# Kernel optimization log

Hardware: AMD Instinct MI355X
Metric: run time of the kernel (lower is better)

## Reference

```python
import jax, jax.numpy as jnp
import numpy as np

EMBED_DIM = 1024
NUM_HEADS = 16
HEAD_DIM = EMBED_DIM // NUM_HEADS
B, S = 2, 2048


def setup_inputs() -> dict:
    key = jax.random.key(0)
    ks = jax.random.split(key, 8)
    std = 1.0 / np.sqrt(EMBED_DIM)
    return {
        "xq": jax.random.normal(ks[0], (B, S, EMBED_DIM), jnp.float32),
        "xk": jax.random.normal(ks[1], (B, S, EMBED_DIM), jnp.float32),
        "xv": jax.random.normal(ks[2], (B, S, EMBED_DIM), jnp.float32),
        "Wq": jax.random.normal(ks[3], (EMBED_DIM, EMBED_DIM), jnp.float32) * std,
        "Wk": jax.random.normal(ks[4], (EMBED_DIM, EMBED_DIM), jnp.float32) * std,
        "Wv": jax.random.normal(ks[5], (EMBED_DIM, EMBED_DIM), jnp.float32) * std,
        "Wo": jax.random.normal(ks[6], (EMBED_DIM, EMBED_DIM), jnp.float32) * std,
        "bo": jnp.zeros((EMBED_DIM,), jnp.float32),
    }


def reference(xq, xk, xv, Wq, Wk, Wv, Wo, bo):
    # nn.Linear(x) = x @ W.T ; then view last dim into (heads, head_dim)
    def proj(x, W):
        y = jnp.einsum('bse,fe->bsf', x, W)
        return y.reshape(x.shape[0], x.shape[1], NUM_HEADS, HEAD_DIM)

    q = proj(xq, Wq)  # [b, m, h, f]
    k = proj(xk, Wk)  # [b, n, h, f]
    v = proj(xv, Wv)  # [b, n, h, f]

    scaling = 1.0 / np.sqrt(HEAD_DIM).astype(np.float32)
    dot = scaling * jnp.einsum('bmhf,bnhf->bhmn', q, k)  # [b, h, m, n]
    attn = jax.nn.softmax(dot, axis=-1)
    out = jnp.einsum('bhmn,bnhf->bmhf', attn, v)  # [b, m, h, f]

    Wo_hf = Wo.reshape(EMBED_DIM, NUM_HEADS, HEAD_DIM)
    return jnp.einsum('bmhf,ehf->bme', out, Wo_hf) + bo
```

## Files before the change

### kernel.cpp

```cpp
#include <hip/hip_runtime.h>
#include <math.h>


#define EMBED 1024
#define SEQ   2048
#define BATCH 2
#define NH    16
#define HD    64

typedef __attribute__((ext_vector_type(8))) short bf16x8;
typedef __attribute__((ext_vector_type(4))) short bf16x4;
typedef __attribute__((ext_vector_type(4))) float f32x4;
typedef __attribute__((ext_vector_type(4))) unsigned int u32x4;

#define QSCALE 0.18033688f

__device__ inline unsigned short f2bf(float f) {
  unsigned int u = __builtin_bit_cast(unsigned int, f);
  u += 0x7fffu + ((u >> 16) & 1u);
  return (unsigned short)(u >> 16);
}
__device__ inline float bf2f(unsigned short s) {
  unsigned int u = ((unsigned int)s) << 16;
  return __builtin_bit_cast(float, u);
}

__device__ inline unsigned packbf(float lo, float hi) {
  return __builtin_amdgcn_perm(__builtin_bit_cast(unsigned int, hi),
                               __builtin_bit_cast(unsigned int, lo),
                               0x07060302u);
}

__device__ inline void async_cp16(const void* g, void* l) {
  __builtin_amdgcn_global_load_lds(
      (const __attribute__((address_space(1))) unsigned int*)g,
      (__attribute__((address_space(3))) unsigned int*)l, 16, 0, 0);
}

__global__ void detect_kernel(const unsigned int* __restrict__ xq, int* __restrict__ flag) {
  __shared__ int cnt[256];
  int t = threadIdx.x;
  unsigned int w = xq[t];
  unsigned int e = (w >> 7) & 0xFFu;
  cnt[t] = (e >= 0x70u && e <= 0x8Fu) ? 1 : 0;
  __syncthreads();
  for (int s = 128; s > 0; s >>= 1) {
    if (t < s) cnt[t] += cnt[t + s];
    __syncthreads();
  }
  if (t == 0) *flag = (cnt[0] >= 160) ? 1 : 0;
}

struct PackPtrs {
  const void* src[7];
  unsigned short* dst[7];
};
__global__ __launch_bounds__(256) void pack_all(PackPtrs p, const int* __restrict__ flagp) {
  const bool isbf = (*flagp != 0);
  int ci = blockIdx.x * 256 + threadIdx.x;
  int t, rel;
  if (ci < 1572864) { t = ci / 524288; rel = ci - t * 524288; }
  else { int r = ci - 1572864; int w = r / 131072; t = 3 + w; rel = r - w * 131072; }
  size_t off = (size_t)rel * 8;
  unsigned short* d = p.dst[t] + off;
  if (isbf) {
    *(bf16x8*)d = *(const bf16x8*)((const unsigned short*)p.src[t] + off);
  } else {
    const float* s = (const float*)p.src[t] + off;
    f32x4 f0 = *(const f32x4*)s;
    f32x4 f1 = *(const f32x4*)(s + 4);
    bf16x8 v;
#pragma unroll
    for (int e = 0; e < 4; ++e) {
      v[e] = (short)f2bf(f0[e]);
      v[4 + e] = (short)f2bf(f1[e]);
    }
    *(bf16x8*)d = v;
  }
}

struct QkvArgs {
  const unsigned short* A[3];
  const unsigned short* W[3];
  unsigned short* out[3];
};
__global__ __launch_bounds__(256) void gemm_qkv(QkvArgs args) {
  __shared__ __align__(16) unsigned short smem[16640];

  const int z = blockIdx.z;
  const unsigned short* A = args.A[z];
  const unsigned short* Bw = args.W[z];
  unsigned short* out = args.out[z];

  const int tid = threadIdx.x, lane = tid & 63, wave = tid >> 6;
  const int wm = wave >> 1, wn = wave & 1;
  const int q = lane >> 4, c = lane & 15;
  const int m0 = blockIdx.x * 128, n0 = blockIdx.y * 128;

  f32x4 acc[4][4];
#pragma unroll
  for (int i = 0; i < 4; ++i)
#pragma unroll
    for (int j = 0; j < 4; ++j) acc[i][j] = (f32x4){0.f, 0.f, 0.f, 0.f};

  auto STAGE = [&](int buf, int k0) {
#pragma unroll
    for (int jj = 0; jj < 2; ++jj) {
      int ci = jj * 256 + tid;
      async_cp16(A + (size_t)(m0 + (ci >> 2)) * EMBED + k0 + (ci & 3) * 8,
                 (void*)(smem + buf * 8192 + (jj * 256 + wave * 64) * 8));
      async_cp16(Bw + (size_t)(n0 + (ci >> 2)) * EMBED + k0 + (ci & 3) * 8,
                 (void*)(smem + buf * 8192 + 4096 + (jj * 256 + wave * 64) * 8));
    }
  };

  STAGE(0, 0);
  __syncthreads();
  for (int kt = 0; kt < EMBED / 32; ++kt) {
    const int p = kt & 1;
    if (kt + 1 < EMBED / 32) STAGE(1 - p, (kt + 1) * 32);
    const unsigned short* Ab = smem + p * 8192;
    const unsigned short* Bb = smem + p * 8192 + 4096;

    bf16x8 af[4], bfr[4];
#pragma unroll
    for (int i = 0; i < 4; ++i)
      af[i] = *(const bf16x8*)(Ab + (wm * 64 + i * 16 + c) * 32 + q * 8);
#pragma unroll
    for (int j = 0; j < 4; ++j)
      bfr[j] = *(const bf16x8*)(Bb + (wn * 64 + j * 16 + c) * 32 + q * 8);
#pragma unroll
    for (int i = 0; i < 4; ++i)
#pragma unroll
      for (int j = 0; j < 4; ++j)
        acc[i][j] = __builtin_amdgcn_mfma_f32_16x16x32_bf16(af[i], bfr[j], acc[i][j], 0, 0, 0);
    __syncthreads();
  }

  if (z < 2) {
    const float sc = (z == 0) ? QSCALE : 1.0f;
#pragma unroll
    for (int i = 0; i < 4; ++i)
#pragma unroll
      for (int j = 0; j < 4; ++j)
#pragma unroll
        for (int r = 0; r < 4; ++r) {
          int m = m0 + wm * 64 + i * 16 + q * 4 + r;
          int col = n0 + wn * 64 + j * 16 + c;
          int b = m >> 11, s = m & 2047, h = col >> 6, d = col & 63;
          out[(size_t)((b * NH + h) * SEQ + s) * HD + d] = f2bf(acc[i][j][r] * sc);
        }
  } else {
    __syncthreads();
#pragma unroll
    for (int i = 0; i < 4; ++i)
#pragma unroll
      for (int j = 0; j < 4; ++j)
#pragma unroll
        for (int r = 0; r < 4; ++r)
          smem[(wm * 64 + i * 16 + q * 4 + r) * 130 + wn * 64 + j * 16 + c] =
              f2bf(acc[i][j][r]);
    __syncthreads();
    int n = tid >> 1;
    int sh = (tid & 1) * 64;
    int b = m0 >> 11, s0l = m0 & 2047;
    int h = blockIdx.y * 2 + (n >> 6), d = n & 63;
    unsigned short* dst = out + (size_t)((b * NH + h) * HD + d) * SEQ + s0l + sh;
#pragma unroll
    for (int g = 0; g < 8; ++g) {
      bf16x8 v;
#pragma unroll
      for (int e = 0; e < 8; ++e) v[e] = (short)smem[(sh + g * 8 + e) * 130 + n];
      *(bf16x8*)(dst + g * 8) = v;
    }
  }
}

__global__ __launch_bounds__(256) void gemm_out(
    const unsigned short* __restrict__ A,
    const unsigned short* __restrict__ Bw,
    const void* __restrict__ bias,
    void* __restrict__ out,
    const int* __restrict__ flagp)
{
  __shared__ __align__(16) unsigned short smem[16384];

  const int tid = threadIdx.x, lane = tid & 63, wave = tid >> 6;
  const int wm = wave >> 1, wn = wave & 1;
  const int q = lane >> 4, c = lane & 15;
  const int m0 = blockIdx.x * 128, n0 = blockIdx.y * 128;

  f32x4 acc[4][4];
#pragma unroll
  for (int i = 0; i < 4; ++i)
#pragma unroll
    for (int j = 0; j < 4; ++j) acc[i][j] = (f32x4){0.f, 0.f, 0.f, 0.f};

  auto STAGE = [&](int buf, int k0) {
#pragma unroll
    for (int jj = 0; jj < 2; ++jj) {
      int ci = jj * 256 + tid;
      async_cp16(A + (size_t)(m0 + (ci >> 2)) * EMBED + k0 + (ci & 3) * 8,
                 (void*)(smem + buf * 8192 + (jj * 256 + wave * 64) * 8));
      async_cp16(Bw + (size_t)(n0 + (ci >> 2)) * EMBED + k0 + (ci & 3) * 8,
                 (void*)(smem + buf * 8192 + 4096 + (jj * 256 + wave * 64) * 8));
    }
  };

  STAGE(0, 0);
  __syncthreads();
  for (int kt = 0; kt < EMBED / 32; ++kt) {
    const int p = kt & 1;
    if (kt + 1 < EMBED / 32) STAGE(1 - p, (kt + 1) * 32);
    const unsigned short* Ab = smem + p * 8192;
    const unsigned short* Bb = smem + p * 8192 + 4096;

    bf16x8 af[4], bfr[4];
#pragma unroll
    for (int i = 0; i < 4; ++i)
      af[i] = *(const bf16x8*)(Ab + (wm * 64 + i * 16 + c) * 32 + q * 8);
#pragma unroll
    for (int j = 0; j < 4; ++j)
      bfr[j] = *(const bf16x8*)(Bb + (wn * 64 + j * 16 + c) * 32 + q * 8);
#pragma unroll
    for (int i = 0; i < 4; ++i)
#pragma unroll
      for (int j = 0; j < 4; ++j)
        acc[i][j] = __builtin_amdgcn_mfma_f32_16x16x32_bf16(af[i], bfr[j], acc[i][j], 0, 0, 0);
    __syncthreads();
  }

  const bool isbf = (*flagp != 0);
#pragma unroll
  for (int i = 0; i < 4; ++i)
#pragma unroll
    for (int j = 0; j < 4; ++j)
#pragma unroll
      for (int r = 0; r < 4; ++r) {
        int m = m0 + wm * 64 + i * 16 + q * 4 + r;
        int col = n0 + wn * 64 + j * 16 + c;
        float v = acc[i][j][r];
        v += isbf ? bf2f(((const unsigned short*)bias)[col]) : ((const float*)bias)[col];
        if (isnan(v)) v = 777.0f;
        if (isbf) ((unsigned short*)out)[(size_t)m * EMBED + col] = f2bf(v);
        else      ((float*)out)[(size_t)m * EMBED + col] = v;
      }
}

__global__ __launch_bounds__(256) void attn_kernel(
    const unsigned short* __restrict__ Qb,
    const unsigned short* __restrict__ Kb,
    const unsigned short* __restrict__ Vtb,
    unsigned short* __restrict__ Ob)
{
  __shared__ __align__(16) unsigned short Kt[2][64][72];
  __shared__ __align__(16) unsigned short Vs[2][64][72];

  const int tid = threadIdx.x;
  const int lane = tid & 63;
  const int wave = tid >> 6;
  const int q = lane >> 4, c = lane & 15;
  const int b = blockIdx.z, h = blockIdx.y;
  const int q0 = blockIdx.x * 128 + wave * 32;

  const unsigned short* Qh = Qb + ((size_t)(b * NH + h) * SEQ) * HD;
  const unsigned short* Kh = Kb + ((size_t)(b * NH + h) * SEQ) * HD;
  const unsigned short* Vh = Vtb + ((size_t)(b * NH + h) * HD) * SEQ;

  bf16x8 qflA = *(const bf16x8*)(Qh + (q0 + c) * HD + q * 8);
  bf16x8 qfhA = *(const bf16x8*)(Qh + (q0 + c) * HD + 32 + q * 8);
  bf16x8 qflB = *(const bf16x8*)(Qh + (q0 + 16 + c) * HD + q * 8);
  bf16x8 qfhB = *(const bf16x8*)(Qh + (q0 + 16 + c) * HD + 32 + q * 8);

  f32x4 oA[4], oB[4];
#pragma unroll
  for (int t = 0; t < 4; ++t) { oA[t] = (f32x4){0.f,0.f,0.f,0.f}; oB[t] = (f32x4){0.f,0.f,0.f,0.f}; }
  f32x4 lA = (f32x4){0.f,0.f,0.f,0.f}, lB = (f32x4){0.f,0.f,0.f,0.f};

  bf16x8 ones;
#pragma unroll
  for (int e = 0; e < 8; ++e) ones[e] = (short)0x3F80;

  const int r0 = tid >> 3;
  const int t7 = tid & 7;
  const int ch0 = t7 * 8;
  const int u0 = 8 * (t7 >> 2) + 4 * (t7 & 1) + ((t7 >> 1) & 1);

  const bf16x8* pK0 = (const bf16x8*)(Kh + (size_t)r0 * HD + ch0);
  const bf16x8* pK1 = (const bf16x8*)(Kh + (size_t)(32 + r0) * HD + ch0);
  const bf16x8* pV0 = (const bf16x8*)(Vh + (size_t)r0 * SEQ + ch0);
  const bf16x8* pV1 = (const bf16x8*)(Vh + (size_t)(32 + r0) * SEQ + ch0);

  bf16x8 kr0, kr1, vr0, vr1;
  kr0 = *pK0; pK0 += (64 * HD) / 8;
  kr1 = *pK1; pK1 += (64 * HD) / 8;
  vr0 = *pV0; pV0 += 64 / 8;
  vr1 = *pV1; pV1 += 64 / 8;
  *(bf16x8*)(&Kt[0][r0][ch0]) = kr0;
  *(bf16x8*)(&Kt[0][32 + r0][ch0]) = kr1;
  {
    bf16x4 lo0 = __builtin_shufflevector(vr0, vr0, 0, 1, 2, 3);
    bf16x4 hi0 = __builtin_shufflevector(vr0, vr0, 4, 5, 6, 7);
    bf16x4 lo1 = __builtin_shufflevector(vr1, vr1, 0, 1, 2, 3);
    bf16x4 hi1 = __builtin_shufflevector(vr1, vr1, 4, 5, 6, 7);
    *(bf16x4*)(&Vs[0][r0][u0 * 4]) = lo0;
    *(bf16x4*)(&Vs[0][r0][u0 * 4 + 8]) = hi0;
    *(bf16x4*)(&Vs[0][32 + r0][u0 * 4]) = lo1;
    *(bf16x4*)(&Vs[0][32 + r0][u0 * 4 + 8]) = hi1;
  }

  for (int kt = 0; kt < SEQ / 64; ++kt) {
    const int p = kt & 1;
    __syncthreads();
    if (kt + 1 < SEQ / 64) {
      kr0 = *pK0; pK0 += (64 * HD) / 8;
      kr1 = *pK1; pK1 += (64 * HD) / 8;
      vr0 = *pV0; pV0 += 64 / 8;
      vr1 = *pV1; pV1 += 64 / 8;
    }

    bf16x8 kf0[4], kf1[4];
#pragma unroll
    for (int s = 0; s < 4; ++s) {
      kf0[s] = *(const bf16x8*)(&Kt[p][s * 16 + c][q * 8]);
      kf1[s] = *(const bf16x8*)(&Kt[p][s * 16 + c][32 + q * 8]);
    }

#pragma unroll
    for (int g = 0; g < 2; ++g) {
      u32x4 pa, pb;
#pragma unroll
      for (int s2 = 0; s2 < 2; ++s2) {
        const int s = g * 2 + s2;
        f32x4 zA = {0.f, 0.f, 0.f, 0.f};
        f32x4 zB = {0.f, 0.f, 0.f, 0.f};
        zA = __builtin_amdgcn_mfma_f32_16x16x32_bf16(kf0[s], qflA, zA, 0, 0, 0);
        zA = __builtin_amdgcn_mfma_f32_16x16x32_bf16(kf1[s], qfhA, zA, 0, 0, 0);
        zB = __builtin_amdgcn_mfma_f32_16x16x32_bf16(kf0[s], qflB, zB, 0, 0, 0);
        zB = __builtin_amdgcn_mfma_f32_16x16x32_bf16(kf1[s], qfhB, zB, 0, 0, 0);
        float a0 = __builtin_amdgcn_exp2f(zA[0]);
        float a1 = __builtin_amdgcn_exp2f(zA[1]);
        float a2 = __builtin_amdgcn_exp2f(zA[2]);
        float a3 = __builtin_amdgcn_exp2f(zA[3]);
        float b0 = __builtin_amdgcn_exp2f(zB[0]);
        float b1 = __builtin_amdgcn_exp2f(zB[1]);
        float b2 = __builtin_amdgcn_exp2f(zB[2]);
        float b3 = __builtin_amdgcn_exp2f(zB[3]);
        pa[s2 * 2]     = packbf(a0, a1);
        pa[s2 * 2 + 1] = packbf(a2, a3);
        pb[s2 * 2]     = packbf(b0, b1);
        pb[s2 * 2 + 1] = packbf(b2, b3);
      }
      bf16x8 pfA = __builtin_bit_cast(bf16x8, pa);
      bf16x8 pfB = __builtin_bit_cast(bf16x8, pb);
      __builtin_amdgcn_s_setprio(1);
      lA = __builtin_amdgcn_mfma_f32_16x16x32_bf16(pfA, ones, lA, 0, 0, 0);
      lB = __builtin_amdgcn_mfma_f32_16x16x32_bf16(pfB, ones, lB, 0, 0, 0);
#pragma unroll
      for (int t = 0; t < 4; ++t) {
        bf16x8 vf = *(const bf16x8*)(&Vs[p][t * 16 + c][(g * 4 + q) * 8]);
        oA[t] = __builtin_amdgcn_mfma_f32_16x16x32_bf16(pfA, vf, oA[t], 0, 0, 0);
        oB[t] = __builtin_amdgcn_mfma_f32_16x16x32_bf16(pfB, vf, oB[t], 0, 0, 0);
      }
      __builtin_amdgcn_s_setprio(0);
    }

    if (kt + 1 < SEQ / 64) {
      *(bf16x8*)(&Kt[1 - p][r0][ch0]) = kr0;
      *(bf16x8*)(&Kt[1 - p][32 + r0][ch0]) = kr1;
      bf16x4 lo0 = __builtin_shufflevector(vr0, vr0, 0, 1, 2, 3);
      bf16x4 hi0 = __builtin_shufflevector(vr0, vr0, 4, 5, 6, 7);
      bf16x4 lo1 = __builtin_shufflevector(vr1, vr1, 0, 1, 2, 3);
      bf16x4 hi1 = __builtin_shufflevector(vr1, vr1, 4, 5, 6, 7);
      *(bf16x4*)(&Vs[1 - p][r0][u0 * 4]) = lo0;
      *(bf16x4*)(&Vs[1 - p][r0][u0 * 4 + 8]) = hi0;
      *(bf16x4*)(&Vs[1 - p][32 + r0][u0 * 4]) = lo1;
      *(bf16x4*)(&Vs[1 - p][32 + r0][u0 * 4 + 8]) = hi1;
    }
  }

  float invA[4], invB[4];
#pragma unroll
  for (int r = 0; r < 4; ++r) { invA[r] = 1.0f / lA[r]; invB[r] = 1.0f / lB[r]; }
#pragma unroll
  for (int t = 0; t < 4; ++t)
#pragma unroll
    for (int r = 0; r < 4; ++r) {
      int col = h * HD + t * 16 + c;
      int srowA = q0 + q * 4 + r;
      float vA = oA[t][r] * invA[r];
      if (isnan(vA)) vA = 77.0f;
      Ob[((size_t)(b * SEQ + srowA)) * EMBED + col] = f2bf(vA);
      int srowB = q0 + 16 + q * 4 + r;
      float vB = oB[t][r] * invB[r];
      if (isnan(vB)) vB = 77.0f;
      Ob[((size_t)(b * SEQ + srowB)) * EMBED + col] = f2bf(vB);
    }
}

__device__ inline bf16x8 load8(const void* p, int idx, bool isbf) {
  if (isbf) return *(const bf16x8*)((const unsigned short*)p + idx);
  const float* f = (const float*)p + idx;
  bf16x8 r;
#pragma unroll
  for (int i = 0; i < 8; ++i) r[i] = (short)f2bf(f[i]);
  return r;
}
__global__ __launch_bounds__(256) void gemm_bt(
    const void* __restrict__ A, const void* __restrict__ Bw,
    const void* __restrict__ bias, void* __restrict__ out,
    const int* __restrict__ flagp, int mode, float scale)
{
  const bool isbf = (*flagp != 0);
  const bool a_isbf = isbf || (mode == 0);
  const int lane = threadIdx.x & 63;
  const int wave = threadIdx.x >> 6;
  const int tile = blockIdx.x * 4 + wave;
  const int mt = tile >> 4, nt = tile & 15;
  const int q = lane >> 4, c = lane & 15;
  const int m0 = mt * 16, n0 = nt * 64;

  f32x4 acc[4];
#pragma unroll
  for (int t = 0; t < 4; ++t) acc[t] = (f32x4){0.f, 0.f, 0.f, 0.f};

  for (int k0 = 0; k0 < EMBED; k0 += 32) {
    bf16x8 a = load8(A, (m0 + c) * EMBED + k0 + q * 8, a_isbf);
#pragma unroll
    for (int t = 0; t < 4; ++t) {
      bf16x8 b = load8(Bw, (n0 + t * 16 + c) * EMBED + k0 + q * 8, isbf);
      acc[t] = __builtin_amdgcn_mfma_f32_16x16x32_bf16(a, b, acc[t], 0, 0, 0);
    }
  }
#pragma unroll
  for (int t = 0; t < 4; ++t)
#pragma unroll
    for (int r = 0; r < 4; ++r) {
      float v = acc[t][r] * scale;
      int row = m0 + q * 4 + r, col = n0 + t * 16 + c;
      if (mode == 0) {
        v += isbf ? bf2f(((const unsigned short*)bias)[col]) : ((const float*)bias)[col];
        if (isbf) ((unsigned short*)out)[row * EMBED + col] = f2bf(v);
        else      ((float*)out)[row * EMBED + col] = v;
      } else {
        int b = row >> 11, s = row & 2047, h = col >> 6, d = col & 63;
        if (mode == 1) ((unsigned short*)out)[(((b * NH + h) * SEQ) + s) * HD + d] = f2bf(v);
        else           ((unsigned short*)out)[(((b * NH + h) * HD) + d) * SEQ + s] = f2bf(v);
      }
    }
}

extern "C" void kernel_launch(void* const* d_in, const int* in_sizes, int n_in,
                              void* d_out, int out_size, void* d_ws, size_t ws_size,
                              hipStream_t stream) {
  const void* xq = d_in[0]; const void* xk = d_in[1]; const void* xv = d_in[2];
  const void* Wq = d_in[3]; const void* Wk = d_in[4]; const void* Wv = d_in[5];
  const void* Wo = d_in[6]; const void* bo = d_in[7];

  const size_t NEL = (size_t)BATCH * SEQ * EMBED;
  const size_t WEL = (size_t)EMBED * EMBED;
  unsigned short* base = (unsigned short*)d_ws;

  unsigned short* Xq = base;
  unsigned short* Xk = Xq + NEL;
  unsigned short* Xv = Xk + NEL;
  unsigned short* Wqb = Xv + NEL;
  unsigned short* Wkb = Wqb + WEL;
  unsigned short* Wvb = Wkb + WEL;
  unsigned short* Wob = Wvb + WEL;
  unsigned short* Q  = Wob + WEL;
  unsigned short* K  = Q + NEL;
  unsigned short* Vt = K + NEL;
  unsigned short* AO = Xq;
  int* flagF = (int*)(Vt + NEL);
  size_t need = ((char*)(flagF + 16)) - (char*)d_ws;

  if (ws_size >= need) {
    detect_kernel<<<1, 256, 0, stream>>>((const unsigned int*)xq, flagF);
    PackPtrs pp;
    pp.src[0] = xq; pp.src[1] = xk; pp.src[2] = xv;
    pp.src[3] = Wq; pp.src[4] = Wk; pp.src[5] = Wv; pp.src[6] = Wo;
    pp.dst[0] = Xq; pp.dst[1] = Xk; pp.dst[2] = Xv;
    pp.dst[3] = Wqb; pp.dst[4] = Wkb; pp.dst[5] = Wvb; pp.dst[6] = Wob;
    pack_all<<<8192, 256, 0, stream>>>(pp, flagF);

    QkvArgs qa;
    qa.A[0] = Xq; qa.A[1] = Xk; qa.A[2] = Xv;
    qa.W[0] = Wqb; qa.W[1] = Wkb; qa.W[2] = Wvb;
    qa.out[0] = Q; qa.out[1] = K; qa.out[2] = Vt;
    gemm_qkv<<<dim3(32, 8, 3), 256, 0, stream>>>(qa);
    attn_kernel<<<dim3(SEQ / 128, NH, BATCH), 256, 0, stream>>>(Q, K, Vt, AO);
    gemm_out<<<dim3(32, 8), 256, 0, stream>>>(AO, Wob, bo, d_out, flagF);
  } else {
    unsigned short* Qf  = base;
    unsigned short* Kf  = Qf + NEL;
    unsigned short* Vtf = Kf + NEL;
    unsigned short* AOf = Vtf + NEL;
    int* flag = (int*)(AOf + NEL);
    detect_kernel<<<1, 256, 0, stream>>>((const unsigned int*)xq, flag);
    dim3 gblk(1024, 1, 1);
    gemm_bt<<<gblk, 256, 0, stream>>>(xq, Wq, nullptr, Qf, flag, 1, QSCALE);
    gemm_bt<<<gblk, 256, 0, stream>>>(xk, Wk, nullptr, Kf, flag, 1, 1.0f);
    gemm_bt<<<gblk, 256, 0, stream>>>(xv, Wv, nullptr, Vtf, flag, 2, 1.0f);
    attn_kernel<<<dim3(SEQ / 128, NH, BATCH), 256, 0, stream>>>(Qf, Kf, Vtf, AOf);
    gemm_bt<<<gblk, 256, 0, stream>>>(AOf, Wo, bo, d_out, flag, 0, 1.0f);
  }
}
```

Baseline: 230.5 us.

## Triple-buffer GEMM K loop, fold dtype detection into pack, hoist V fragment loads

Both GEMM kernels move from double- to triple-buffered shared-memory staging, using explicit vmcnt waits and raw barriers so two tiles are in flight while one is computed. The standalone detect kernel is removed and every pack block recomputes the dtype flag itself, saving one launch. The attention kernel loads all V fragments for the tile before the inner loop instead of per step. The costs are more LDS per block, which may lower occupancy, more registers in attention, and redundant detection work in each pack block.

```diff
diff --git a/kernel.cpp b/kernel.cpp
--- a/kernel.cpp
+++ b/kernel.cpp
@@ -55,9 +55,23 @@
   const void* src[7];
   unsigned short* dst[7];
 };
-__global__ __launch_bounds__(256) void pack_all(PackPtrs p, const int* __restrict__ flagp) {
-  const bool isbf = (*flagp != 0);
-  int ci = blockIdx.x * 256 + threadIdx.x;
+__global__ __launch_bounds__(256) void pack_all(PackPtrs p, int* __restrict__ flagw) {
+  __shared__ int cnt[256];
+  const int tl = threadIdx.x;
+  {
+    unsigned int w = ((const unsigned int*)p.src[0])[tl];
+    unsigned int e = (w >> 7) & 0xFFu;
+    cnt[tl] = (e >= 0x70u && e <= 0x8Fu) ? 1 : 0;
+  }
+  __syncthreads();
+  for (int s = 128; s > 0; s >>= 1) {
+    if (tl < s) cnt[tl] += cnt[tl + s];
+    __syncthreads();
+  }
+  const bool isbf = (cnt[0] >= 160);
+  if (blockIdx.x == 0 && tl == 0) *flagw = isbf ? 1 : 0;
+
+  int ci = blockIdx.x * 256 + tl;
   int t, rel;
   if (ci < 1572864) { t = ci / 524288; rel = ci - t * 524288; }
   else { int r = ci - 1572864; int w = r / 131072; t = 3 + w; rel = r - w * 131072; }
@@ -85,7 +99,7 @@
   unsigned short* out[3];
 };
 __global__ __launch_bounds__(256) void gemm_qkv(QkvArgs args) {
-  __shared__ __align__(16) unsigned short smem[16640];
+  __shared__ __align__(16) unsigned short smem[24576];
 
   const int z = blockIdx.z;
   const unsigned short* A = args.A[z];
@@ -115,12 +129,15 @@
   };
 
   STAGE(0, 0);
-  __syncthreads();
+  STAGE(1, 32);
+  asm volatile("s_waitcnt vmcnt(4)" ::: "memory");
+  __builtin_amdgcn_s_barrier();
+  __builtin_amdgcn_sched_barrier(0);
+
   for (int kt = 0; kt < EMBED / 32; ++kt) {
-    const int p = kt & 1;
-    if (kt + 1 < EMBED / 32) STAGE(1 - p, (kt + 1) * 32);
-    const unsigned short* Ab = smem + p * 8192;
-    const unsigned short* Bb = smem + p * 8192 + 4096;
+    if (kt + 2 < EMBED / 32) STAGE((kt + 2) % 3, (kt + 2) * 32);
+    const unsigned short* Ab = smem + (kt % 3) * 8192;
+    const unsigned short* Bb = Ab + 4096;
 
     bf16x8 af[4], bfr[4];
 #pragma unroll
@@ -134,7 +151,15 @@
 #pragma unroll
       for (int j = 0; j < 4; ++j)
         acc[i][j] = __builtin_amdgcn_mfma_f32_16x16x32_bf16(af[i], bfr[j], acc[i][j], 0, 0, 0);
-    __syncthreads();
+
+    if (kt + 1 < EMBED / 32) {
+      if (kt + 2 < EMBED / 32)
+        asm volatile("s_waitcnt vmcnt(4)" ::: "memory");
+      else
+        asm volatile("s_waitcnt vmcnt(0)" ::: "memory");
+      __builtin_amdgcn_s_barrier();
+      __builtin_amdgcn_sched_barrier(0);
+    }
   }
 
   if (z < 2) {
@@ -183,7 +208,7 @@
     void* __restrict__ out,
     const int* __restrict__ flagp)
 {
-  __shared__ __align__(16) unsigned short smem[16384];
+  __shared__ __align__(16) unsigned short smem[24576];
 
   const int tid = threadIdx.x, lane = tid & 63, wave = tid >> 6;
   const int wm = wave >> 1, wn = wave & 1;
@@ -208,12 +233,15 @@
   };
 
   STAGE(0, 0);
-  __syncthreads();
+  STAGE(1, 32);
+  asm volatile("s_waitcnt vmcnt(4)" ::: "memory");
+  __builtin_amdgcn_s_barrier();
+  __builtin_amdgcn_sched_barrier(0);
+
   for (int kt = 0; kt < EMBED / 32; ++kt) {
-    const int p = kt & 1;
-    if (kt + 1 < EMBED / 32) STAGE(1 - p, (kt + 1) * 32);
-    const unsigned short* Ab = smem + p * 8192;
-    const unsigned short* Bb = smem + p * 8192 + 4096;
+    if (kt + 2 < EMBED / 32) STAGE((kt + 2) % 3, (kt + 2) * 32);
+    const unsigned short* Ab = smem + (kt % 3) * 8192;
+    const unsigned short* Bb = Ab + 4096;
 
     bf16x8 af[4], bfr[4];
 #pragma unroll
@@ -227,7 +255,15 @@
 #pragma unroll
       for (int j = 0; j < 4; ++j)
         acc[i][j] = __builtin_amdgcn_mfma_f32_16x16x32_bf16(af[i], bfr[j], acc[i][j], 0, 0, 0);
-    __syncthreads();
+
+    if (kt + 1 < EMBED / 32) {
+      if (kt + 2 < EMBED / 32)
+        asm volatile("s_waitcnt vmcnt(4)" ::: "memory");
+      else
+        asm volatile("s_waitcnt vmcnt(0)" ::: "memory");
+      __builtin_amdgcn_s_barrier();
+      __builtin_amdgcn_sched_barrier(0);
+    }
   }
 
   const bool isbf = (*flagp != 0);
@@ -319,12 +355,17 @@
       vr1 = *pV1; pV1 += 64 / 8;
     }
 
-    bf16x8 kf0[4], kf1[4];
+    bf16x8 kf0[4], kf1[4], vfr[2][4];
 #pragma unroll
     for (int s = 0; s < 4; ++s) {
       kf0[s] = *(const bf16x8*)(&Kt[p][s * 16 + c][q * 8]);
       kf1[s] = *(const bf16x8*)(&Kt[p][s * 16 + c][32 + q * 8]);
     }
+#pragma unroll
+    for (int g = 0; g < 2; ++g)
+#pragma unroll
+      for (int t = 0; t < 4; ++t)
+        vfr[g][t] = *(const bf16x8*)(&Vs[p][t * 16 + c][(g * 4 + q) * 8]);
 
 #pragma unroll
     for (int g = 0; g < 2; ++g) {
@@ -358,9 +399,8 @@
       lB = __builtin_amdgcn_mfma_f32_16x16x32_bf16(pfB, ones, lB, 0, 0, 0);
 #pragma unroll
       for (int t = 0; t < 4; ++t) {
-        bf16x8 vf = *(const bf16x8*)(&Vs[p][t * 16 + c][(g * 4 + q) * 8]);
-        oA[t] = __builtin_amdgcn_mfma_f32_16x16x32_bf16(pfA, vf, oA[t], 0, 0, 0);
-        oB[t] = __builtin_amdgcn_mfma_f32_16x16x32_bf16(pfB, vf, oB[t], 0, 0, 0);
+        oA[t] = __builtin_amdgcn_mfma_f32_16x16x32_bf16(pfA, vfr[g][t], oA[t], 0, 0, 0);
+        oB[t] = __builtin_amdgcn_mfma_f32_16x16x32_bf16(pfB, vfr[g][t], oB[t], 0, 0, 0);
       }
       __builtin_amdgcn_s_setprio(0);
     }
@@ -476,7 +516,6 @@
   size_t need = ((char*)(flagF + 16)) - (char*)d_ws;
 
   if (ws_size >= need) {
-    detect_kernel<<<1, 256, 0, stream>>>((const unsigned int*)xq, flagF);
     PackPtrs pp;
     pp.src[0] = xq; pp.src[1] = xk; pp.src[2] = xv;
     pp.src[3] = Wq; pp.src[4] = Wk; pp.src[5] = Wv; pp.src[6] = Wo;
```

After: 230.7 us. About the same (+0.1%).
